# Kernel optimization log

Measured on AMD Instinct MI355X. Metric: run time of the kernel, lower is better.

Reference implementation:

```python
import jax, jax.numpy as jnp
import numpy as np

EMBED_DIM = 1024
NUM_HEADS = 16
HEAD_DIM = EMBED_DIM // NUM_HEADS
SCALE = HEAD_DIM ** -0.5
T, B = 1024, 4
NEG_INF = -1e9


def setup_inputs() -> dict:
    key = jax.random.key(0)
    k1, k2, k3 = jax.random.split(key, 3)
    query = jax.random.normal(k1, (T, B, EMBED_DIM), dtype=jnp.float32)
    # xavier-ish init scale for weights
    in_proj_weight = jax.random.normal(k2, (3 * EMBED_DIM, EMBED_DIM), dtype=jnp.float32) * 0.02
    in_proj_bias = jnp.zeros((3 * EMBED_DIM,), dtype=jnp.float32)
    out_w = jax.random.normal(k3, (EMBED_DIM, EMBED_DIM), dtype=jnp.float32) * 0.02
    out_b = jnp.zeros((EMBED_DIM,), dtype=jnp.float32)
    # pad the last quarter of key positions; causal mask guarantees every
    # query row still sees at least one unmasked key
    key_padding_mask = jnp.broadcast_to(jnp.arange(T) >= (3 * T) // 4, (B, T))
    return {
        "query": query,
        "key_padding_mask": key_padding_mask,
        "in_proj_weight": in_proj_weight,
        "in_proj_bias": in_proj_bias,
        "out_w": out_w,
        "out_b": out_b,
    }


def reference(query, key_padding_mask, in_proj_weight, in_proj_bias, out_w, out_b):
    tgt_len, bsz, _ = query.shape
    src_len = tgt_len  # self-attention (qkv_same path)
    # in_proj: F.linear(x, W, b) = x @ W.T + b -> [T, B, 3E]
    qkv = jnp.einsum("tbe,fe->tbf", query, in_proj_weight) + in_proj_bias
    q, k, v = jnp.split(qkv, 3, axis=-1)
    q = q * SCALE
    # reshape to [T, B, H, d]
    q = q.reshape(tgt_len, bsz, NUM_HEADS, HEAD_DIM)
    k = k.reshape(src_len, bsz, NUM_HEADS, HEAD_DIM)
    v = v.reshape(src_len, bsz, NUM_HEADS, HEAD_DIM)
    # scores [B, H, T, S]
    scores = jnp.einsum("tbhd,sbhd->bhts", q, k)
    # mask_future_timesteps=True: additive upper-triangular -inf mask
    causal = jnp.triu(jnp.full((tgt_len, src_len), NEG_INF, dtype=scores.dtype), 1)
    scores = scores + causal
    # key padding mask: [B, S] -> broadcast over heads and tgt positions
    scores = jnp.where(key_padding_mask[:, None, None, :], NEG_INF, scores)
    attn_weights = jax.nn.softmax(scores.astype(jnp.float32), axis=-1).astype(scores.dtype)
    # dropout p=0 / eval mode -> identity
    attn = jnp.einsum("bhts,sbhd->tbhd", attn_weights, v)
    attn = attn.reshape(tgt_len, bsz, EMBED_DIM)
    attn = jnp.einsum("tbe,fe->tbf", attn, out_w) + out_b
    avg_weights = attn_weights.mean(axis=1)  # [B, T, S]
    return attn, avg_weights
```

## Files before the change

kernel.cpp:

```cpp
#include <hip/hip_runtime.h>
#include <hip/hip_bf16.h>

#define SCALE_Q 0.125f
#define S_PAD  768

typedef __bf16 bf16x8 __attribute__((ext_vector_type(8)));
typedef __bf16 bf16x4 __attribute__((ext_vector_type(4)));
typedef float  f32x4  __attribute__((ext_vector_type(4)));
using bf16 = __hip_bfloat16;

__device__ inline bf16x4 cvt4(const float* __restrict__ p) {
    f32x4 v = *reinterpret_cast<const f32x4*>(p);
    bf16x4 r;
    r[0] = (__bf16)v[0]; r[1] = (__bf16)v[1]; r[2] = (__bf16)v[2]; r[3] = (__bf16)v[3];
    return r;
}

__device__ inline void gll16(const void* gsrc, void* ldst) {
    __builtin_amdgcn_global_load_lds(
        (const __attribute__((address_space(1))) unsigned int*)gsrc,
        (__attribute__((address_space(3))) unsigned int*)ldst,
        16, 0, 0);
}

__global__ __launch_bounds__(256) void convert_bf16(
    const float* __restrict__ x, const float* __restrict__ w,
    __bf16* __restrict__ xb, __bf16* __restrict__ wb)
{
    const int idx = blockIdx.x * 256 + threadIdx.x;
    if (idx < 1048576) {
        f32x4 v = reinterpret_cast<const f32x4*>(x)[idx];
        bf16x4 r;
        r[0] = (__bf16)v[0]; r[1] = (__bf16)v[1];
        r[2] = (__bf16)v[2]; r[3] = (__bf16)v[3];
        reinterpret_cast<bf16x4*>(xb)[idx] = r;
    } else {
        const int j = idx - 1048576;
        f32x4 v = reinterpret_cast<const f32x4*>(w)[j];
        bf16x4 r;
        r[0] = (__bf16)v[0]; r[1] = (__bf16)v[1];
        r[2] = (__bf16)v[2]; r[3] = (__bf16)v[3];
        reinterpret_cast<bf16x4*>(wb)[j] = r;
    }
}

__global__ __launch_bounds__(256) void qkv_proj(
    const __bf16* __restrict__ xb,
    const __bf16* __restrict__ wb,
    const float* __restrict__ bias,
    bf16* __restrict__ qh, bf16* __restrict__ kh, bf16* __restrict__ vt)
{
    __shared__ __bf16 As[128 * 64];
    __shared__ __bf16 Bs[128 * 64];
    const int tid  = threadIdx.x;
    const int lane = tid & 63, wave = tid >> 6;
    const int l15  = lane & 15, q = lane >> 4;
    const int wm   = wave >> 1, wn = wave & 1;
    const int m0   = (blockIdx.x / 24) * 128;
    const int n0   = (blockIdx.x % 24) * 128;

    const int srow = lane >> 3;
    const int scol = (lane & 7) * 8;

    f32x4 acc[4][4];
#pragma unroll
    for (int i = 0; i < 4; ++i)
#pragma unroll
        for (int j = 0; j < 4; ++j) acc[i][j] = (f32x4){0.f, 0.f, 0.f, 0.f};

    for (int k0 = 0; k0 < 1024; k0 += 64) {
        __syncthreads();
#pragma unroll
        for (int j = 0; j < 4; ++j) {
            const int c   = wave * 4 + j;
            const int row = c * 8 + srow;
            gll16(&xb[(size_t)(m0 + row) * 1024 + k0 + scol], &As[c * 512]);
            gll16(&wb[(size_t)(n0 + row) * 1024 + k0 + scol], &Bs[c * 512]);
        }
        __syncthreads();
#pragma unroll
        for (int kk = 0; kk < 2; ++kk) {
            bf16x8 af[4], bfr[4];
#pragma unroll
            for (int i = 0; i < 4; ++i)
                af[i] = *reinterpret_cast<const bf16x8*>(
                    &As[(wm * 64 + i * 16 + l15) * 64 + kk * 32 + q * 8]);
#pragma unroll
            for (int j = 0; j < 4; ++j)
                bfr[j] = *reinterpret_cast<const bf16x8*>(
                    &Bs[(wn * 64 + j * 16 + l15) * 64 + kk * 32 + q * 8]);
#pragma unroll
            for (int i = 0; i < 4; ++i)
#pragma unroll
                for (int j = 0; j < 4; ++j)
                    acc[i][j] = __builtin_amdgcn_mfma_f32_16x16x32_bf16(
                        af[i], bfr[j], acc[i][j], 0, 0, 0);
        }
    }

#pragma unroll
    for (int j = 0; j < 4; ++j) {
        const int n = n0 + wn * 64 + j * 16 + l15;
        const float bv = bias[n];
        const int which = n >> 10;
        const int e = n & 1023;
        const int h = e >> 6, d = e & 63;
        const float sc = (which == 0) ? SCALE_Q : 1.0f;
#pragma unroll
        for (int i = 0; i < 4; ++i) {
#pragma unroll
            for (int rr = 0; rr < 4; ++rr) {
                const int m = m0 + wm * 64 + i * 16 + q * 4 + rr;
                const int t = m >> 2, b = m & 3;
                bf16 val = __float2bfloat16((acc[i][j][rr] + bv) * sc);
                if (which == 0)      qh[(((b * 16 + h) * 1024 + t) * 64) + d] = val;
                else if (which == 1) kh[(((b * 16 + h) * 1024 + t) * 64) + d] = val;
                else                 vt[(((b * 16 + h) * 64 + d) * 1024) + t] = val;
            }
        }
    }
}

#define PSTRIDE 120
__global__ __launch_bounds__(512, 1) void attn_kernel(
    const bf16* __restrict__ qh, const bf16* __restrict__ kh,
    const bf16* __restrict__ vt,
    bf16* __restrict__ ctx,
    float* __restrict__ avg_out)
{
    const int tid  = threadIdx.x;
    const int wave = tid >> 6, lane = tid & 63;
    const int l15  = lane & 15, q = lane >> 4;
    const int t0   = blockIdx.x * 16;
    const int b    = blockIdx.y;
    const int t_glob = t0 + l15;
    const int ntiles = min(t0 / 16 + 1, 48);
    const int nt_w = (wave < ntiles) ? ((ntiles - 1 - wave) >> 3) + 1 : 0;
    const int npair = (nt_w + 1) >> 1;
    const int voff  = (q & 1) * 8;

    __shared__ __bf16 Plds[8][16 * PSTRIDE];
    __shared__ float  obuf[8][16][64];
    __shared__ float2 redml[8][16];

    f32x4 avg_acc[6];
#pragma unroll
    for (int r = 0; r < 6; ++r) avg_acc[r] = (f32x4){0.f, 0.f, 0.f, 0.f};

    bf16x8 qf0, qf1, kf[6][2], vf[3][4];
    {
        const int bh = b * 16;
        const bf16* qp = qh + ((size_t)(bh * 1024 + t_glob)) * 64 + q * 8;
        qf0 = *reinterpret_cast<const bf16x8*>(qp);
        qf1 = *reinterpret_cast<const bf16x8*>(qp + 32);
#pragma unroll
        for (int r = 0; r < 6; ++r) {
            if (r < nt_w) {
                const bf16* kp = kh + ((size_t)(bh * 1024 + (wave + 8 * r) * 16 + l15)) * 64 + q * 8;
                kf[r][0] = *reinterpret_cast<const bf16x8*>(kp);
                kf[r][1] = *reinterpret_cast<const bf16x8*>(kp + 32);
            }
        }
#pragma unroll
        for (int rp = 0; rp < 3; ++rp) {
            if (rp < npair) {
                const int sl   = rp * 2 + (q >> 1);
                const int scol = (wave + 8 * sl) * 16 + voff;
#pragma unroll
                for (int n = 0; n < 4; ++n)
                    vf[rp][n] = *reinterpret_cast<const bf16x8*>(
                        vt + ((size_t)(bh * 64 + n * 16 + l15)) * 1024 + scol);
            }
        }
    }

    for (int h = 0; h < 16; ++h) {
        const int bh  = b * 16 + h;
        const int bhn = bh + 1;

        f32x4 acc[6];
        float lm = -1e30f;
#pragma unroll
        for (int r = 0; r < 6; ++r) {
            if (r < nt_w) {
                const int tile = wave + 8 * r;
                f32x4 c = {0.f, 0.f, 0.f, 0.f};
                c = __builtin_amdgcn_mfma_f32_16x16x32_bf16(kf[r][0], qf0, c, 0, 0, 0);
                c = __builtin_amdgcn_mfma_f32_16x16x32_bf16(kf[r][1], qf1, c, 0, 0, 0);
#pragma unroll
                for (int i = 0; i < 4; ++i) {
                    int s = tile * 16 + q * 4 + i;
                    bool valid = (s <= t_glob) && (s < S_PAD);
                    float v = valid ? c[i] : -1e30f;
                    c[i] = v;
                    lm = fmaxf(lm, v);
                }
                acc[r] = c;
            }
        }

        bf16x8 qn0 = qf0, qn1 = qf1;
        if (h < 15) {
#pragma unroll
            for (int r = 0; r < 6; ++r) {
                if (r < nt_w) {
                    const bf16* kp = kh + ((size_t)(bhn * 1024 + (wave + 8 * r) * 16 + l15)) * 64 + q * 8;
                    kf[r][0] = *reinterpret_cast<const bf16x8*>(kp);
                    kf[r][1] = *reinterpret_cast<const bf16x8*>(kp + 32);
                }
            }
            const bf16* qp = qh + ((size_t)(bhn * 1024 + t_glob)) * 64 + q * 8;
            qn0 = *reinterpret_cast<const bf16x8*>(qp);
            qn1 = *reinterpret_cast<const bf16x8*>(qp + 32);
        }

        lm = fmaxf(lm, __shfl_xor(lm, 16));
        lm = fmaxf(lm, __shfl_xor(lm, 32));
        const float m_w = lm;

        float ls = 0.f;
#pragma unroll
        for (int r = 0; r < 6; ++r) {
            if (r < nt_w) {
#pragma unroll
                for (int i = 0; i < 4; ++i) {
                    float e = __expf(acc[r][i] - m_w);
                    acc[r][i] = e;
                    ls += e;
                }
            }
        }
        ls += __shfl_xor(ls, 16);
        ls += __shfl_xor(ls, 32);
        if (q == 0) redml[wave][l15] = make_float2(m_w, ls);
        __syncthreads();

        float m = -1e30f;
#pragma unroll
        for (int i = 0; i < 8; ++i) m = fmaxf(m, redml[i][l15].x);
        float L = 0.f;
#pragma unroll
        for (int i = 0; i < 8; ++i) {
            float2 ml = redml[i][l15];
            L += ml.y * __expf(ml.x - m);
        }
        const float scale = __expf(m_w - m) / L;

        __bf16* pw = &Plds[wave][l15 * PSTRIDE];
#pragma unroll
        for (int r = 0; r < 6; ++r) {
            if (r < nt_w) {
                bf16x4 pk;
#pragma unroll
                for (int i = 0; i < 4; ++i) {
                    float pn = acc[r][i] * scale;
                    avg_acc[r][i] += pn * 0.0625f;
                    pk[i] = (__bf16)pn;
                }
                *reinterpret_cast<bf16x4*>(pw + r * 16 + q * 4) = pk;
            }
        }
        if (nt_w < 7)
            *reinterpret_cast<bf16x4*>(pw + nt_w * 16 + q * 4) = (bf16x4){};

        f32x4 o[4];
#pragma unroll
        for (int n = 0; n < 4; ++n) o[n] = (f32x4){0.f, 0.f, 0.f, 0.f};
#pragma unroll
        for (int rp = 0; rp < 3; ++rp) {
            if (rp < npair) {
                const int sl = rp * 2 + (q >> 1);
                bf16x8 pa = *reinterpret_cast<const bf16x8*>(
                    &Plds[wave][l15 * PSTRIDE + sl * 16 + voff]);
#pragma unroll
                for (int n = 0; n < 4; ++n)
                    o[n] = __builtin_amdgcn_mfma_f32_16x16x32_bf16(pa, vf[rp][n], o[n], 0, 0, 0);
            }
        }

        if (h < 15) {
#pragma unroll
            for (int rp = 0; rp < 3; ++rp) {
                if (rp < npair) {
                    const int sl   = rp * 2 + (q >> 1);
                    const int scol = (wave + 8 * sl) * 16 + voff;
#pragma unroll
                    for (int n = 0; n < 4; ++n)
                        vf[rp][n] = *reinterpret_cast<const bf16x8*>(
                            vt + ((size_t)(bhn * 64 + n * 16 + l15)) * 1024 + scol);
                }
            }
        }

#pragma unroll
        for (int n = 0; n < 4; ++n)
#pragma unroll
            for (int i = 0; i < 4; ++i)
                obuf[wave][q * 4 + i][n * 16 + l15] = o[n][i];
        __syncthreads();

#pragma unroll
        for (int j = 0; j < 2; ++j) {
            int idx = tid + j * 512;
            int t = idx >> 6, d = idx & 63;
            float val = 0.f;
#pragma unroll
            for (int wv = 0; wv < 8; ++wv) val += obuf[wv][t][d];
            ctx[((size_t)((t0 + t) * 4 + b)) * 1024 + h * 64 + d] = __float2bfloat16(val);
        }

        qf0 = qn0; qf1 = qn1;
    }

    float* ao = avg_out + ((size_t)(b * 1024 + t_glob)) * 1024;
    const f32x4 zero = {0.f, 0.f, 0.f, 0.f};
#pragma unroll
    for (int r = 0; r < 8; ++r) {
        const int tile = wave + 8 * r;
        f32x4 v = zero;
        if (r < 6 && r < nt_w) v = avg_acc[r];
        *reinterpret_cast<f32x4*>(ao + tile * 16 + q * 4) = v;
    }
}

__global__ __launch_bounds__(256) void out_proj(
    const bf16* __restrict__ ctxm,
    const float* __restrict__ w,
    const float* __restrict__ bias,
    float* __restrict__ out)
{
    __shared__ __bf16 As[128 * 64];
    __shared__ __bf16 Bs[128 * 64];
    const int tid  = threadIdx.x;
    const int lane = tid & 63, wave = tid >> 6;
    const int l15  = lane & 15, q = lane >> 4;
    const int wm   = wave >> 1, wn = wave & 1;
    const int m0   = (blockIdx.x / 8) * 128;
    const int n0   = (blockIdx.x % 8) * 128;

    const int srow  = lane >> 3;
    const int scol  = (lane & 7) * 8;
    const int srowB = tid >> 4;
    const int scolB = (tid & 15) * 4;

    f32x4 acc[4][4];
#pragma unroll
    for (int i = 0; i < 4; ++i)
#pragma unroll
        for (int j = 0; j < 4; ++j) acc[i][j] = (f32x4){0.f, 0.f, 0.f, 0.f};

    for (int k0 = 0; k0 < 1024; k0 += 64) {
        __syncthreads();
#pragma unroll
        for (int j = 0; j < 4; ++j) {
            const int c   = wave * 4 + j;
            const int row = c * 8 + srow;
            gll16(&ctxm[(size_t)(m0 + row) * 1024 + k0 + scol], &As[c * 512]);
        }
#pragma unroll
        for (int r = 0; r < 8; ++r) {
            int row = r * 16 + srowB;
            *reinterpret_cast<bf16x4*>(&Bs[row * 64 + scolB]) =
                cvt4(&w[(size_t)(n0 + row) * 1024 + k0 + scolB]);
        }
        __syncthreads();
#pragma unroll
        for (int kk = 0; kk < 2; ++kk) {
            bf16x8 af[4], bfr[4];
#pragma unroll
            for (int i = 0; i < 4; ++i)
                af[i] = *reinterpret_cast<const bf16x8*>(
                    &As[(wm * 64 + i * 16 + l15) * 64 + kk * 32 + q * 8]);
#pragma unroll
            for (int j = 0; j < 4; ++j)
                bfr[j] = *reinterpret_cast<const bf16x8*>(
                    &Bs[(wn * 64 + j * 16 + l15) * 64 + kk * 32 + q * 8]);
#pragma unroll
            for (int i = 0; i < 4; ++i)
#pragma unroll
                for (int j = 0; j < 4; ++j)
                    acc[i][j] = __builtin_amdgcn_mfma_f32_16x16x32_bf16(
                        af[i], bfr[j], acc[i][j], 0, 0, 0);
        }
    }

#pragma unroll
    for (int j = 0; j < 4; ++j) {
        const int n = n0 + wn * 64 + j * 16 + l15;
        const float bv = bias[n];
#pragma unroll
        for (int i = 0; i < 4; ++i) {
#pragma unroll
            for (int rr = 0; rr < 4; ++rr) {
                const int m = m0 + wm * 64 + i * 16 + q * 4 + rr;
                out[(size_t)m * 1024 + n] = acc[i][j][rr] + bv;
            }
        }
    }
}

extern "C" void kernel_launch(void* const* d_in, const int* in_sizes, int n_in,
                              void* d_out, int out_size, void* d_ws, size_t ws_size,
                              hipStream_t stream) {
    const float* query = (const float*)d_in[0];
    const float* w_in  = (const float*)d_in[2];
    const float* b_in  = (const float*)d_in[3];
    const float* w_out = (const float*)d_in[4];
    const float* b_out = (const float*)d_in[5];

    float* out0 = (float*)d_out;
    float* avg  = out0 + (size_t)4 * 1024 * 1024;

    bf16* qh  = (bf16*)d_ws;
    bf16* kh  = qh + (size_t)4 * 1024 * 1024;
    bf16* vt  = kh + (size_t)4 * 1024 * 1024;
    bf16* ctx = vt + (size_t)4 * 1024 * 1024;

    __bf16* xb = (__bf16*)avg;
    __bf16* wb = xb + (size_t)4 * 1024 * 1024;

    convert_bf16<<<dim3(7168), dim3(256), 0, stream>>>(query, w_in, xb, wb);
    qkv_proj<<<dim3(32 * 24), dim3(256), 0, stream>>>(xb, wb, b_in, qh, kh, vt);
    attn_kernel<<<dim3(64, 4), dim3(512), 0, stream>>>(qh, kh, vt, ctx, avg);
    out_proj<<<dim3(32 * 8), dim3(256), 0, stream>>>(ctx, w_out, b_out, out0);
}
```

Measured before the change: 287.7 us.

## Double-buffer LDS tiles in QKV and output projection GEMMs

Both projection GEMMs now keep two LDS buffers per operand and prefetch the next K-tile while MFMAs run on the current one, dropping one of the two barriers per iteration. The aim is to hide global-load latency behind compute. In the attention kernel, two __syncthreads are replaced by an explicit lgkmcnt wait plus s_barrier, which avoids waiting on outstanding vector-memory loads. LDS use per block doubles to 64KB, which can lower occupancy. The out_proj prefetch converts fp32 to bf16 synchronously through registers, so its overlap is limited.

```diff
diff --git a/kernel.cpp b/kernel.cpp
--- a/kernel.cpp
+++ b/kernel.cpp
@@ -21,6 +21,11 @@
         (const __attribute__((address_space(1))) unsigned int*)gsrc,
         (__attribute__((address_space(3))) unsigned int*)ldst,
         16, 0, 0);
+}
+
+__device__ inline void bar_lgkm() {
+    asm volatile("s_waitcnt lgkmcnt(0)" ::: "memory");
+    __builtin_amdgcn_s_barrier();
 }
 
 __global__ __launch_bounds__(256) void convert_bf16(
@@ -50,8 +55,8 @@
     const float* __restrict__ bias,
     bf16* __restrict__ qh, bf16* __restrict__ kh, bf16* __restrict__ vt)
 {
-    __shared__ __bf16 As[128 * 64];
-    __shared__ __bf16 Bs[128 * 64];
+    __shared__ __bf16 As[2][128 * 64];
+    __shared__ __bf16 Bs[2][128 * 64];
     const int tid  = threadIdx.x;
     const int lane = tid & 63, wave = tid >> 6;
     const int l15  = lane & 15, q = lane >> 4;
@@ -68,27 +73,39 @@
 #pragma unroll
         for (int j = 0; j < 4; ++j) acc[i][j] = (f32x4){0.f, 0.f, 0.f, 0.f};
 
-    for (int k0 = 0; k0 < 1024; k0 += 64) {
-        __syncthreads();
-#pragma unroll
-        for (int j = 0; j < 4; ++j) {
-            const int c   = wave * 4 + j;
-            const int row = c * 8 + srow;
-            gll16(&xb[(size_t)(m0 + row) * 1024 + k0 + scol], &As[c * 512]);
-            gll16(&wb[(size_t)(n0 + row) * 1024 + k0 + scol], &Bs[c * 512]);
-        }
-        __syncthreads();
+#pragma unroll
+    for (int j = 0; j < 4; ++j) {
+        const int c   = wave * 4 + j;
+        const int row = c * 8 + srow;
+        gll16(&xb[(size_t)(m0 + row) * 1024 + scol], &As[0][c * 512]);
+        gll16(&wb[(size_t)(n0 + row) * 1024 + scol], &Bs[0][c * 512]);
+    }
+    __syncthreads();
+
+    int cur = 0;
+    for (int t = 0; t < 16; ++t) {
+        const int nxt = cur ^ 1;
+        if (t < 15) {
+            const int k0 = (t + 1) * 64;
+#pragma unroll
+            for (int j = 0; j < 4; ++j) {
+                const int c   = wave * 4 + j;
+                const int row = c * 8 + srow;
+                gll16(&xb[(size_t)(m0 + row) * 1024 + k0 + scol], &As[nxt][c * 512]);
+                gll16(&wb[(size_t)(n0 + row) * 1024 + k0 + scol], &Bs[nxt][c * 512]);
+            }
+        }
 #pragma unroll
         for (int kk = 0; kk < 2; ++kk) {
             bf16x8 af[4], bfr[4];
 #pragma unroll
             for (int i = 0; i < 4; ++i)
                 af[i] = *reinterpret_cast<const bf16x8*>(
-                    &As[(wm * 64 + i * 16 + l15) * 64 + kk * 32 + q * 8]);
+                    &As[cur][(wm * 64 + i * 16 + l15) * 64 + kk * 32 + q * 8]);
 #pragma unroll
             for (int j = 0; j < 4; ++j)
                 bfr[j] = *reinterpret_cast<const bf16x8*>(
-                    &Bs[(wn * 64 + j * 16 + l15) * 64 + kk * 32 + q * 8]);
+                    &Bs[cur][(wn * 64 + j * 16 + l15) * 64 + kk * 32 + q * 8]);
 #pragma unroll
             for (int i = 0; i < 4; ++i)
 #pragma unroll
@@ -96,6 +113,8 @@
                     acc[i][j] = __builtin_amdgcn_mfma_f32_16x16x32_bf16(
                         af[i], bfr[j], acc[i][j], 0, 0, 0);
         }
+        if (t < 15) __syncthreads();
+        cur = nxt;
     }
 
 #pragma unroll
@@ -233,7 +252,7 @@
         ls += __shfl_xor(ls, 16);
         ls += __shfl_xor(ls, 32);
         if (q == 0) redml[wave][l15] = make_float2(m_w, ls);
-        __syncthreads();
+        bar_lgkm();
 
         float m = -1e30f;
 #pragma unroll
@@ -297,7 +316,7 @@
 #pragma unroll
             for (int i = 0; i < 4; ++i)
                 obuf[wave][q * 4 + i][n * 16 + l15] = o[n][i];
-        __syncthreads();
+        bar_lgkm();
 
 #pragma unroll
         for (int j = 0; j < 2; ++j) {
@@ -329,8 +348,8 @@
     const float* __restrict__ bias,
     float* __restrict__ out)
 {
-    __shared__ __bf16 As[128 * 64];
-    __shared__ __bf16 Bs[128 * 64];
+    __shared__ __bf16 As[2][128 * 64];
+    __shared__ __bf16 Bs[2][128 * 64];
     const int tid  = threadIdx.x;
     const int lane = tid & 63, wave = tid >> 6;
     const int l15  = lane & 15, q = lane >> 4;
@@ -349,32 +368,49 @@
 #pragma unroll
         for (int j = 0; j < 4; ++j) acc[i][j] = (f32x4){0.f, 0.f, 0.f, 0.f};
 
-    for (int k0 = 0; k0 < 1024; k0 += 64) {
-        __syncthreads();
-#pragma unroll
-        for (int j = 0; j < 4; ++j) {
-            const int c   = wave * 4 + j;
-            const int row = c * 8 + srow;
-            gll16(&ctxm[(size_t)(m0 + row) * 1024 + k0 + scol], &As[c * 512]);
-        }
-#pragma unroll
-        for (int r = 0; r < 8; ++r) {
-            int row = r * 16 + srowB;
-            *reinterpret_cast<bf16x4*>(&Bs[row * 64 + scolB]) =
-                cvt4(&w[(size_t)(n0 + row) * 1024 + k0 + scolB]);
-        }
-        __syncthreads();
+#pragma unroll
+    for (int j = 0; j < 4; ++j) {
+        const int c   = wave * 4 + j;
+        const int row = c * 8 + srow;
+        gll16(&ctxm[(size_t)(m0 + row) * 1024 + scol], &As[0][c * 512]);
+    }
+#pragma unroll
+    for (int r = 0; r < 8; ++r) {
+        int row = r * 16 + srowB;
+        *reinterpret_cast<bf16x4*>(&Bs[0][row * 64 + scolB]) =
+            cvt4(&w[(size_t)(n0 + row) * 1024 + scolB]);
+    }
+    __syncthreads();
+
+    int cur = 0;
+    for (int t = 0; t < 16; ++t) {
+        const int nxt = cur ^ 1;
+        if (t < 15) {
+            const int k0 = (t + 1) * 64;
+#pragma unroll
+            for (int j = 0; j < 4; ++j) {
+                const int c   = wave * 4 + j;
+                const int row = c * 8 + srow;
+                gll16(&ctxm[(size_t)(m0 + row) * 1024 + k0 + scol], &As[nxt][c * 512]);
+            }
+#pragma unroll
+            for (int r = 0; r < 8; ++r) {
+                int row = r * 16 + srowB;
+                *reinterpret_cast<bf16x4*>(&Bs[nxt][row * 64 + scolB]) =
+                    cvt4(&w[(size_t)(n0 + row) * 1024 + k0 + scolB]);
+            }
+        }
 #pragma unroll
         for (int kk = 0; kk < 2; ++kk) {
             bf16x8 af[4], bfr[4];
 #pragma unroll
             for (int i = 0; i < 4; ++i)
                 af[i] = *reinterpret_cast<const bf16x8*>(
-                    &As[(wm * 64 + i * 16 + l15) * 64 + kk * 32 + q * 8]);
+                    &As[cur][(wm * 64 + i * 16 + l15) * 64 + kk * 32 + q * 8]);
 #pragma unroll
             for (int j = 0; j < 4; ++j)
                 bfr[j] = *reinterpret_cast<const bf16x8*>(
-                    &Bs[(wn * 64 + j * 16 + l15) * 64 + kk * 32 + q * 8]);
+                    &Bs[cur][(wn * 64 + j * 16 + l15) * 64 + kk * 32 + q * 8]);
 #pragma unroll
             for (int i = 0; i < 4; ++i)
 #pragma unroll
@@ -382,6 +418,8 @@
                     acc[i][j] = __builtin_amdgcn_mfma_f32_16x16x32_bf16(
                         af[i], bfr[j], acc[i][j], 0, 0, 0);
         }
+        if (t < 15) __syncthreads();
+        cur = nxt;
     }
 
 #pragma unroll
```

Result: slower. 297.3 us (+3.3%).

## Tile V-transpose layout, remap attention blocks to XCDs, use lgkm-only barriers

Applied to the files above, without the earlier changes.

The transposed V buffer is stored in 16-token tiles, so each tile's 64x16 slab is contiguous and the attention kernel's V fragment loads touch one compact 2 KB region instead of 64 rows strided by 1024 elements. The attention grid is flattened to 1D, and block IDs are remapped so each batch's query tiles land on the same pair of XCDs, which should improve L2 reuse of K/V. The two __syncthreads calls are replaced with an lgkmcnt-only wait plus s_barrier, so outstanding global V prefetches need not drain at each barrier. The last change depends on the global prefetch results not being read across the barrier before they arrive.

```diff
diff --git a/kernel.cpp b/kernel.cpp
--- a/kernel.cpp
+++ b/kernel.cpp
@@ -21,6 +21,11 @@
         (const __attribute__((address_space(1))) unsigned int*)gsrc,
         (__attribute__((address_space(3))) unsigned int*)ldst,
         16, 0, 0);
+}
+
+__device__ inline void bar_lgkm() {
+    asm volatile("s_waitcnt lgkmcnt(0)" ::: "memory");
+    __builtin_amdgcn_s_barrier();
 }
 
 __global__ __launch_bounds__(256) void convert_bf16(
@@ -115,7 +120,8 @@
                 bf16 val = __float2bfloat16((acc[i][j][rr] + bv) * sc);
                 if (which == 0)      qh[(((b * 16 + h) * 1024 + t) * 64) + d] = val;
                 else if (which == 1) kh[(((b * 16 + h) * 1024 + t) * 64) + d] = val;
-                else                 vt[(((b * 16 + h) * 64 + d) * 1024) + t] = val;
+                else                 vt[(((size_t)(b * 16 + h)) << 16)
+                                        + ((t >> 4) * 1024) + (d * 16) + (t & 15)] = val;
             }
         }
     }
@@ -131,8 +137,11 @@
     const int tid  = threadIdx.x;
     const int wave = tid >> 6, lane = tid & 63;
     const int l15  = lane & 15, q = lane >> 4;
-    const int t0   = blockIdx.x * 16;
-    const int b    = blockIdx.y;
+    const int bid  = blockIdx.x;
+    const int xcd  = bid & 7;
+    const int b    = xcd >> 1;
+    const int t0i  = ((bid >> 3) << 1) | (xcd & 1);
+    const int t0   = t0i * 16;
     const int t_glob = t0 + l15;
     const int ntiles = min(t0 / 16 + 1, 48);
     const int nt_w = (wave < ntiles) ? ((ntiles - 1 - wave) >> 3) + 1 : 0;
@@ -161,15 +170,16 @@
                 kf[r][1] = *reinterpret_cast<const bf16x8*>(kp + 32);
             }
         }
+        const bf16* vb0 = vt + ((size_t)bh << 16);
 #pragma unroll
         for (int rp = 0; rp < 3; ++rp) {
             if (rp < npair) {
                 const int sl   = rp * 2 + (q >> 1);
-                const int scol = (wave + 8 * sl) * 16 + voff;
+                const int tile = wave + 8 * sl;
 #pragma unroll
                 for (int n = 0; n < 4; ++n)
                     vf[rp][n] = *reinterpret_cast<const bf16x8*>(
-                        vt + ((size_t)(bh * 64 + n * 16 + l15)) * 1024 + scol);
+                        vb0 + tile * 1024 + (n * 16 + l15) * 16 + voff);
             }
         }
     }
@@ -233,7 +243,7 @@
         ls += __shfl_xor(ls, 16);
         ls += __shfl_xor(ls, 32);
         if (q == 0) redml[wave][l15] = make_float2(m_w, ls);
-        __syncthreads();
+        bar_lgkm();
 
         float m = -1e30f;
 #pragma unroll
@@ -279,15 +289,16 @@
         }
 
         if (h < 15) {
+            const bf16* vbn = vt + ((size_t)bhn << 16);
 #pragma unroll
             for (int rp = 0; rp < 3; ++rp) {
                 if (rp < npair) {
                     const int sl   = rp * 2 + (q >> 1);
-                    const int scol = (wave + 8 * sl) * 16 + voff;
+                    const int tile = wave + 8 * sl;
 #pragma unroll
                     for (int n = 0; n < 4; ++n)
                         vf[rp][n] = *reinterpret_cast<const bf16x8*>(
-                            vt + ((size_t)(bhn * 64 + n * 16 + l15)) * 1024 + scol);
+                            vbn + tile * 1024 + (n * 16 + l15) * 16 + voff);
                 }
             }
         }
@@ -297,7 +308,7 @@
 #pragma unroll
             for (int i = 0; i < 4; ++i)
                 obuf[wave][q * 4 + i][n * 16 + l15] = o[n][i];
-        __syncthreads();
+        bar_lgkm();
 
 #pragma unroll
         for (int j = 0; j < 2; ++j) {
@@ -421,6 +432,6 @@
 
     convert_bf16<<<dim3(7168), dim3(256), 0, stream>>>(query, w_in, xb, wb);
     qkv_proj<<<dim3(32 * 24), dim3(256), 0, stream>>>(xb, wb, b_in, qh, kh, vt);
-    attn_kernel<<<dim3(64, 4), dim3(512), 0, stream>>>(qh, kh, vt, ctx, avg);
+    attn_kernel<<<dim3(256), dim3(512), 0, stream>>>(qh, kh, vt, ctx, avg);
     out_proj<<<dim3(32 * 8), dim3(256), 0, stream>>>(ctx, w_out, b_out, out0);
 }
```

After: 272.9 us. -5.1%, faster.
